# Performance work log

Hardware: AMD Instinct MI355X
Metric: run time of the kernel (lower is better)

The kernel has to match this reference:

```python
import jax, jax.numpy as jnp
import numpy as np

LAG = 1  # from init_kwargs

def _from_embedding(z, lag):
    # torch loop: out[i] = z[i] for i < lag; out[i] = z[i] + detach(out[i-lag]) otherwise.
    # For i grouped by residue class mod lag this is a cumulative sum along dim 0.
    # The detach means gradients flow only through the direct z[i] term (identity grad),
    # so forward = cumsum, and we restore detach semantics with stop_gradient.
    N = z.shape[0]
    assert N % lag == 0, "sequence length must be a multiple of lag"
    zg = z.reshape(N // lag, lag, *z.shape[1:])        # [G, lag, B, D]
    cum = jnp.cumsum(zg, axis=0).reshape(z.shape)       # [N, B, D]
    # forward value = cum; backward: d(out)/d(z) = identity (accumulated prefix detached)
    return jax.lax.stop_gradient(cum - z) + z

def setup_inputs() -> dict:
    key = jax.random.key(0)
    k1, = jax.random.split(key, 1)
    z = jax.random.normal(k1, (8192, 64, 128), dtype=jnp.float32)
    previous_loss = jnp.zeros((1,), dtype=jnp.float32)
    return {"z": z, "previous_loss": previous_loss}

def reference(z, previous_loss):
    z_delagged = _from_embedding(z, LAG)
    return (z_delagged, previous_loss)
```

## Files before the change

### kernel.cpp

```cpp
#include <hip/hip_runtime.h>


typedef float f4 __attribute__((ext_vector_type(4)));

constexpr int NROWS = 8192;
constexpr int NCOLS = 8192;
constexpr int NCOL4 = NCOLS / 4;
constexpr int TPB   = 256;
constexpr int KCH   = 128;
constexpr int RR    = NROWS / KCH;
constexpr int CT    = NCOL4 / TPB;

__global__ __launch_bounds__(TPB) void k_partial(const f4* __restrict__ z,
                                                 f4* __restrict__ part) {
    const int tile  = blockIdx.x & (CT - 1);
    const int chunk = blockIdx.x >> 3;
    const int c4    = tile * TPB + threadIdx.x;
    const f4* p = z + (size_t)chunk * RR * NCOL4 + c4;
    f4 a = (f4)0.f;
    #pragma unroll 8
    for (int r = 0; r < RR; ++r) a += p[(size_t)r * NCOL4];
    part[(size_t)chunk * NCOL4 + c4] = a;
}

__global__ __launch_bounds__(TPB) void k_scan(float* __restrict__ part,
                                              const float* __restrict__ prev,
                                              float* __restrict__ out_tail) {
    const int c = blockIdx.x * TPB + threadIdx.x;
    float run = 0.f;
    #pragma unroll 16
    for (int k = 0; k < KCH; ++k) {
        const size_t i = (size_t)k * NCOLS + c;
        float v = part[i];
        part[i] = run;
        run += v;
    }
    if (blockIdx.x == 0 && threadIdx.x == 0) out_tail[0] = prev[0];
}

__global__ __launch_bounds__(TPB) void k_apply(const f4* __restrict__ z,
                                               const f4* __restrict__ part,
                                               f4* __restrict__ out) {
    const int tile  = blockIdx.x & (CT - 1);
    const int chunk = KCH - 1 - (blockIdx.x >> 3);
    const int c4    = tile * TPB + threadIdx.x;
    f4 a = part[(size_t)chunk * NCOL4 + c4];
    const f4* p = z   + (size_t)chunk * RR * NCOL4 + c4;
    f4*       q = out + (size_t)chunk * RR * NCOL4 + c4;
    #pragma unroll 4
    for (int r = 0; r < RR; ++r) {
        a += p[(size_t)r * NCOL4];
        __builtin_nontemporal_store(a, &q[(size_t)r * NCOL4]);
    }
}

extern "C" void kernel_launch(void* const* d_in, const int* in_sizes, int n_in,
                              void* d_out, int out_size, void* d_ws, size_t ws_size,
                              hipStream_t stream) {
    const f4*    z    = (const f4*)d_in[0];
    const float* prev = (const float*)d_in[1];
    float*       out  = (float*)d_out;
    float*       part = (float*)d_ws;
    float*       tail = out + (size_t)NROWS * NCOLS;

    k_partial<<<KCH * CT, TPB, 0, stream>>>(z, (f4*)part);
    k_scan<<<NCOLS / TPB, TPB, 0, stream>>>(part, prev, tail);
    k_apply<<<KCH * CT, TPB, 0, stream>>>(z, (const f4*)part, (f4*)out);
}
```

Measured before the change: 136.6 us.

## Fuse three-pass chunked cumsum into one cooperative kernel with grid syncs

Replaces the partial-sum, scan and apply kernels with a single cooperative kernel. Each thread keeps its 32-row chunk's running prefix in registers, writes the chunk total, and a grid sync lets 8 blocks scan the totals before another grid sync. Every thread then adds its prefix and writes the output, so the input is read once instead of twice. The costs are two grid-wide barriers, a serial 256-step scan done by only 8 blocks, and high register pressure under the 8-blocks-per-CU launch bound, which may cause spills. The old three-kernel path remains as a fallback when the occupancy check fails.

```diff
diff --git a/kernel.cpp b/kernel.cpp
--- a/kernel.cpp
+++ b/kernel.cpp
@@ -1,4 +1,7 @@
 #include <hip/hip_runtime.h>
+#include <hip/hip_cooperative_groups.h>
+
+namespace cg = cooperative_groups;
 
 
 typedef float f4 __attribute__((ext_vector_type(4)));
@@ -7,9 +10,55 @@
 constexpr int NCOLS = 8192;
 constexpr int NCOL4 = NCOLS / 4;
 constexpr int TPB   = 256;
-constexpr int KCH   = 128;
-constexpr int RR    = NROWS / KCH;
-constexpr int CT    = NCOL4 / TPB;
+
+constexpr int FK    = 256;
+constexpr int FR    = NROWS / FK;
+constexpr int FT    = NCOL4 / TPB;
+constexpr int FGRID = FK * FT;
+
+__global__ __launch_bounds__(TPB, 8) void k_fused(
+    const f4* __restrict__ z, f4* __restrict__ out, f4* __restrict__ agg,
+    const float* __restrict__ prev, float* __restrict__ out_tail)
+{
+    const int bid   = blockIdx.x;
+    const int chunk = bid >> 3;
+    const int tile  = bid & (FT - 1);
+    const int tid   = threadIdx.x;
+    const int c4    = tile * TPB + tid;
+
+    if (bid == 0 && tid == 0) out_tail[0] = prev[0];
+
+    const f4* p = z + (size_t)chunk * FR * NCOL4 + c4;
+    f4 v[FR];
+    f4 run = (f4)0.f;
+    #pragma unroll
+    for (int r = 0; r < FR; ++r) { run += p[(size_t)r * NCOL4]; v[r] = run; }
+    agg[(size_t)chunk * NCOL4 + c4] = run;
+
+    __threadfence();
+    cg::this_grid().sync();
+
+    if (bid < FT) {
+        const int col = bid * TPB + tid;
+        f4 s = (f4)0.f;
+        #pragma unroll 8
+        for (int k = 0; k < FK; ++k) {
+            const size_t i = (size_t)k * NCOL4 + col;
+            f4 t = agg[i]; agg[i] = s; s += t;
+        }
+    }
+    __threadfence();
+    cg::this_grid().sync();
+
+    const f4 prefix = agg[(size_t)chunk * NCOL4 + c4];
+    f4* q = out + (size_t)chunk * FR * NCOL4 + c4;
+    #pragma unroll
+    for (int r = 0; r < FR; ++r) q[(size_t)r * NCOL4] = v[r] + prefix;
+}
+
+constexpr int KCH = 128;
+constexpr int RR  = NROWS / KCH;
+constexpr int CT  = NCOL4 / TPB;
 
 __global__ __launch_bounds__(TPB) void k_partial(const f4* __restrict__ z,
                                                  f4* __restrict__ part) {
@@ -60,9 +109,28 @@
     const f4*    z    = (const f4*)d_in[0];
     const float* prev = (const float*)d_in[1];
     float*       out  = (float*)d_out;
-    float*       part = (float*)d_ws;
     float*       tail = out + (size_t)NROWS * NCOLS;
 
+    const size_t agg_bytes = (size_t)FK * NCOL4 * sizeof(f4);
+
+    int blocksPerCU = 0;
+    hipError_t qe = hipOccupancyMaxActiveBlocksPerMultiprocessor(
+        &blocksPerCU, (const void*)k_fused, TPB, 0);
+    const bool coop_ok = (qe == hipSuccess) && (blocksPerCU >= FGRID / 256) &&
+                         (ws_size >= agg_bytes);
+
+    if (coop_ok) {
+        f4* agg = (f4*)d_ws;
+        f4* outv = (f4*)out;
+        void* args[] = { (void*)&z, (void*)&outv, (void*)&agg,
+                         (void*)&prev, (void*)&tail };
+        hipError_t le = hipLaunchCooperativeKernel((const void*)k_fused,
+                                                   dim3(FGRID), dim3(TPB),
+                                                   args, 0, stream);
+        if (le == hipSuccess) return;
+    }
+
+    float* part = (float*)d_ws;
     k_partial<<<KCH * CT, TPB, 0, stream>>>(z, (f4*)part);
     k_scan<<<NCOLS / TPB, TPB, 0, stream>>>(part, prev, tail);
     k_apply<<<KCH * CT, TPB, 0, stream>>>(z, (const f4*)part, (f4*)out);
```

New measurement: 136.0 us. About the same (-0.4%).

## Split columns into two panels so apply pass re-reads z from cache

Applied to the files above, without the earlier changes.

Runs the partial-sum, scan and apply kernels separately on each half of the columns, so each panel's z footprint (half the tensor) can stay in the last-level cache between the partial and apply passes. This aims to cut the second full HBM read of z. The apply chunk order changes from reverse to forward, and unroll factors are raised. It adds three extra kernel launches and halves the per-launch grid size.

```diff
diff --git a/kernel.cpp b/kernel.cpp
--- a/kernel.cpp
+++ b/kernel.cpp
@@ -3,30 +3,36 @@
 
 typedef float f4 __attribute__((ext_vector_type(4)));
 
-constexpr int NROWS = 8192;
-constexpr int NCOLS = 8192;
-constexpr int NCOL4 = NCOLS / 4;
-constexpr int TPB   = 256;
-constexpr int KCH   = 128;
-constexpr int RR    = NROWS / KCH;
-constexpr int CT    = NCOL4 / TPB;
+constexpr int NROWS  = 8192;
+constexpr int NCOLS  = 8192;
+constexpr int NCOL4  = NCOLS / 4;
+constexpr int TPB    = 256;
+constexpr int KCH    = 128;
+constexpr int RR     = NROWS / KCH;
+
+constexpr int NPAN   = 2;
+constexpr int PANW4  = NCOL4 / NPAN;
+constexpr int PT     = PANW4 / TPB;
+constexpr int PGRID  = KCH * PT;
 
 __global__ __launch_bounds__(TPB) void k_partial(const f4* __restrict__ z,
-                                                 f4* __restrict__ part) {
-    const int tile  = blockIdx.x & (CT - 1);
-    const int chunk = blockIdx.x >> 3;
-    const int c4    = tile * TPB + threadIdx.x;
+                                                 f4* __restrict__ part,
+                                                 int colBase4) {
+    const int tile  = blockIdx.x & (PT - 1);
+    const int chunk = blockIdx.x / PT;
+    const int c4    = colBase4 + tile * TPB + threadIdx.x;
     const f4* p = z + (size_t)chunk * RR * NCOL4 + c4;
     f4 a = (f4)0.f;
-    #pragma unroll 8
+    #pragma unroll 16
     for (int r = 0; r < RR; ++r) a += p[(size_t)r * NCOL4];
     part[(size_t)chunk * NCOL4 + c4] = a;
 }
 
 __global__ __launch_bounds__(TPB) void k_scan(float* __restrict__ part,
+                                              int colBaseF,
                                               const float* __restrict__ prev,
                                               float* __restrict__ out_tail) {
-    const int c = blockIdx.x * TPB + threadIdx.x;
+    const int c = colBaseF + blockIdx.x * TPB + threadIdx.x;
     float run = 0.f;
     #pragma unroll 16
     for (int k = 0; k < KCH; ++k) {
@@ -35,19 +41,21 @@
         part[i] = run;
         run += v;
     }
-    if (blockIdx.x == 0 && threadIdx.x == 0) out_tail[0] = prev[0];
+    if (colBaseF == 0 && blockIdx.x == 0 && threadIdx.x == 0)
+        out_tail[0] = prev[0];
 }
 
 __global__ __launch_bounds__(TPB) void k_apply(const f4* __restrict__ z,
                                                const f4* __restrict__ part,
-                                               f4* __restrict__ out) {
-    const int tile  = blockIdx.x & (CT - 1);
-    const int chunk = KCH - 1 - (blockIdx.x >> 3);
-    const int c4    = tile * TPB + threadIdx.x;
+                                               f4* __restrict__ out,
+                                               int colBase4) {
+    const int tile  = blockIdx.x & (PT - 1);
+    const int chunk = blockIdx.x / PT;
+    const int c4    = colBase4 + tile * TPB + threadIdx.x;
     f4 a = part[(size_t)chunk * NCOL4 + c4];
     const f4* p = z   + (size_t)chunk * RR * NCOL4 + c4;
     f4*       q = out + (size_t)chunk * RR * NCOL4 + c4;
-    #pragma unroll 4
+    #pragma unroll 8
     for (int r = 0; r < RR; ++r) {
         a += p[(size_t)r * NCOL4];
         __builtin_nontemporal_store(a, &q[(size_t)r * NCOL4]);
@@ -63,7 +71,11 @@
     float*       part = (float*)d_ws;
     float*       tail = out + (size_t)NROWS * NCOLS;
 
-    k_partial<<<KCH * CT, TPB, 0, stream>>>(z, (f4*)part);
-    k_scan<<<NCOLS / TPB, TPB, 0, stream>>>(part, prev, tail);
-    k_apply<<<KCH * CT, TPB, 0, stream>>>(z, (const f4*)part, (f4*)out);
+    for (int pan = 0; pan < NPAN; ++pan) {
+        const int colBase4 = pan * PANW4;
+        const int colBaseF = colBase4 * 4;
+        k_partial<<<PGRID, TPB, 0, stream>>>(z, (f4*)part, colBase4);
+        k_scan<<<(PANW4 * 4) / TPB, TPB, 0, stream>>>(part, colBaseF, prev, tail);
+        k_apply<<<PGRID, TPB, 0, stream>>>(z, (const f4*)part, (f4*)out, colBase4);
+    }
 }
```

After: 192.4 us. +40.9%, slower.

## Fuse three-pass scan into one kernel with inter-block flag synchronization

Applied to the files above, without the earlier changes.

Replaces the partial-sum, scan and apply kernels with a single kernel. Each block reduces its chunk, publishes its aggregate with a release flag, then spin-waits on the flags of earlier chunks in the same column tile and sums their aggregates to form its prefix before writing outputs. This removes two kernel launches and the separate scan pass. It relies on all 512 blocks being co-resident or scheduled in order to avoid deadlock, and adds a memset of the flags plus spin-wait latency. Each chunk's z slice is still read twice.

```diff
diff --git a/kernel.cpp b/kernel.cpp
--- a/kernel.cpp
+++ b/kernel.cpp
@@ -7,19 +7,77 @@
 constexpr int NCOLS = 8192;
 constexpr int NCOL4 = NCOLS / 4;
 constexpr int TPB   = 256;
-constexpr int KCH   = 128;
-constexpr int RR    = NROWS / KCH;
-constexpr int CT    = NCOL4 / TPB;
+
+constexpr int KCH   = 64;
+constexpr int R     = NROWS / KCH;
+constexpr int NTILE = NCOL4 / TPB;
+constexpr int GRID  = KCH * NTILE;
+
+__global__ __launch_bounds__(TPB) void k_onepass(
+    const f4* __restrict__ z, f4* __restrict__ out,
+    f4* __restrict__ agg, unsigned int* __restrict__ flags,
+    const float* __restrict__ prev, float* __restrict__ out_tail)
+{
+    const int bid   = blockIdx.x;
+    const int chunk = bid >> 3;
+    const int tile  = bid & (NTILE - 1);
+    const int tid   = threadIdx.x;
+    const int c4    = tile * TPB + tid;
+
+    if (bid == 0 && tid == 0) out_tail[0] = prev[0];
+
+    const f4* p = z + (size_t)chunk * R * NCOL4 + c4;
+
+    f4 a = (f4)0.f;
+    #pragma unroll 16
+    for (int r = 0; r < R; ++r) a += p[(size_t)r * NCOL4];
+
+    const int slot = tile * KCH + chunk;
+    agg[(size_t)slot * TPB + tid] = a;
+    __threadfence();
+    __syncthreads();
+    if (tid == 0)
+        __hip_atomic_store(&flags[slot], 1u, __ATOMIC_RELEASE,
+                           __HIP_MEMORY_SCOPE_AGENT);
+
+    f4 prefix = (f4)0.f;
+    if (chunk > 0) {
+        if (tid < chunk) {
+            const int fs = tile * KCH + tid;
+            while (__hip_atomic_load(&flags[fs], __ATOMIC_RELAXED,
+                                     __HIP_MEMORY_SCOPE_AGENT) == 0u)
+                __builtin_amdgcn_s_sleep(8);
+        }
+        __syncthreads();
+        __builtin_amdgcn_fence(__ATOMIC_ACQUIRE, "agent");
+        const f4* ap = agg + (size_t)tile * KCH * TPB + tid;
+        #pragma unroll 4
+        for (int cp = 0; cp < chunk; ++cp)
+            prefix += ap[(size_t)cp * TPB];
+    }
+
+    f4* q = out + (size_t)chunk * R * NCOL4 + c4;
+    f4 s = prefix;
+    #pragma unroll 8
+    for (int r = 0; r < R; ++r) {
+        s += p[(size_t)r * NCOL4];
+        __builtin_nontemporal_store(s, &q[(size_t)r * NCOL4]);
+    }
+}
+
+constexpr int FKCH = 128;
+constexpr int FRR  = NROWS / FKCH;
+constexpr int FCT  = NCOL4 / TPB;
 
 __global__ __launch_bounds__(TPB) void k_partial(const f4* __restrict__ z,
                                                  f4* __restrict__ part) {
-    const int tile  = blockIdx.x & (CT - 1);
+    const int tile  = blockIdx.x & (FCT - 1);
     const int chunk = blockIdx.x >> 3;
     const int c4    = tile * TPB + threadIdx.x;
-    const f4* p = z + (size_t)chunk * RR * NCOL4 + c4;
+    const f4* p = z + (size_t)chunk * FRR * NCOL4 + c4;
     f4 a = (f4)0.f;
     #pragma unroll 8
-    for (int r = 0; r < RR; ++r) a += p[(size_t)r * NCOL4];
+    for (int r = 0; r < FRR; ++r) a += p[(size_t)r * NCOL4];
     part[(size_t)chunk * NCOL4 + c4] = a;
 }
 
@@ -29,7 +87,7 @@
     const int c = blockIdx.x * TPB + threadIdx.x;
     float run = 0.f;
     #pragma unroll 16
-    for (int k = 0; k < KCH; ++k) {
+    for (int k = 0; k < FKCH; ++k) {
         const size_t i = (size_t)k * NCOLS + c;
         float v = part[i];
         part[i] = run;
@@ -41,14 +99,14 @@
 __global__ __launch_bounds__(TPB) void k_apply(const f4* __restrict__ z,
                                                const f4* __restrict__ part,
                                                f4* __restrict__ out) {
-    const int tile  = blockIdx.x & (CT - 1);
-    const int chunk = KCH - 1 - (blockIdx.x >> 3);
+    const int tile  = blockIdx.x & (FCT - 1);
+    const int chunk = FKCH - 1 - (blockIdx.x >> 3);
     const int c4    = tile * TPB + threadIdx.x;
     f4 a = part[(size_t)chunk * NCOL4 + c4];
-    const f4* p = z   + (size_t)chunk * RR * NCOL4 + c4;
-    f4*       q = out + (size_t)chunk * RR * NCOL4 + c4;
+    const f4* p = z   + (size_t)chunk * FRR * NCOL4 + c4;
+    f4*       q = out + (size_t)chunk * FRR * NCOL4 + c4;
     #pragma unroll 4
-    for (int r = 0; r < RR; ++r) {
+    for (int r = 0; r < FRR; ++r) {
         a += p[(size_t)r * NCOL4];
         __builtin_nontemporal_store(a, &q[(size_t)r * NCOL4]);
     }
@@ -60,10 +118,20 @@
     const f4*    z    = (const f4*)d_in[0];
     const float* prev = (const float*)d_in[1];
     float*       out  = (float*)d_out;
-    float*       part = (float*)d_ws;
     float*       tail = out + (size_t)NROWS * NCOLS;
 
-    k_partial<<<KCH * CT, TPB, 0, stream>>>(z, (f4*)part);
-    k_scan<<<NCOLS / TPB, TPB, 0, stream>>>(part, prev, tail);
-    k_apply<<<KCH * CT, TPB, 0, stream>>>(z, (const f4*)part, (f4*)out);
+    const size_t agg_bytes  = (size_t)GRID * TPB * sizeof(f4);
+    const size_t flag_bytes = (size_t)GRID * sizeof(unsigned int);
+
+    if (ws_size >= agg_bytes + flag_bytes) {
+        f4* agg = (f4*)d_ws;
+        unsigned int* flags = (unsigned int*)((char*)d_ws + agg_bytes);
+        hipMemsetAsync(flags, 0, flag_bytes, stream);
+        k_onepass<<<GRID, TPB, 0, stream>>>(z, (f4*)out, agg, flags, prev, tail);
+    } else {
+        float* part = (float*)d_ws;
+        k_partial<<<FKCH * FCT, TPB, 0, stream>>>(z, (f4*)part);
+        k_scan<<<NCOLS / TPB, TPB, 0, stream>>>(part, prev, tail);
+        k_apply<<<FKCH * FCT, TPB, 0, stream>>>(z, (const f4*)part, (f4*)out);
+    }
 }
```

Result: slower. 230.7 us (+68.9%).
